# Kernel optimization log

Hardware: AMD Instinct MI355X
Metric: run time of the kernel (lower is better)

## Reference

```python
import jax, jax.numpy as jnp
import numpy as np

E, H, I, T = 8, 1024, 2816, 8192  # experts, hidden, intermediate, total tokens


def setup_inputs() -> dict:
    key = jax.random.key(0)
    k1, k2, k3, k4 = jax.random.split(key, 4)
    x = jax.random.normal(k1, (T, H), dtype=jnp.float32)
    # xavier_normal std = sqrt(2 / (fan_in + fan_out))
    std = (2.0 / (H + I)) ** 0.5
    gate = jax.random.normal(k2, (E, H, I), dtype=jnp.float32) * std
    up = jax.random.normal(k3, (E, H, I), dtype=jnp.float32) * std
    down = jax.random.normal(k4, (E, I, H), dtype=jnp.float32) * std
    # tokens are pre-permuted so each expert's tokens are contiguous; equal split here
    tokens_per_expert = jnp.full((E,), T // E, dtype=jnp.int32)
    return {
        "permuted_local_hidden_states": x,
        "grouped_gate_proj": gate,
        "grouped_up_proj": up,
        "grouped_down_proj": down,
        "tokens_per_expert": tokens_per_expert,
    }


def reference(permuted_local_hidden_states, grouped_gate_proj, grouped_up_proj,
              grouped_down_proj, tokens_per_expert):
    # grouped GEMM: for expert e, rows in its contiguous segment are multiplied by W[e]
    o1 = jax.lax.ragged_dot(permuted_local_hidden_states, grouped_gate_proj,
                            tokens_per_expert)            # [T, I]
    o2 = jax.lax.ragged_dot(permuted_local_hidden_states, grouped_up_proj,
                            tokens_per_expert)            # [T, I]
    inter = jax.nn.silu(o1) * o2                          # SwiGLU  [T, I]
    out = jax.lax.ragged_dot(inter, grouped_down_proj, tokens_per_expert)  # [T, H]
    return out
```

## Files before the change

kernel.cpp:

```cpp
#include <hip/hip_runtime.h>
#include <hip/hip_bf16.h>


#define E_ 8
#define H_ 1024
#define I_ 2816
#define T_ 8192

typedef unsigned short u16;
typedef __attribute__((ext_vector_type(8))) short s16x8;
typedef __attribute__((ext_vector_type(8))) unsigned short u16x8;
typedef __attribute__((ext_vector_type(4))) float f32x4;

__device__ __forceinline__ void async16(const u16* g, u16* l) {
  __builtin_amdgcn_global_load_lds((__attribute__((address_space(1))) void*)g,
                                   (__attribute__((address_space(3))) void*)l, 16, 0, 0);
}

__device__ __forceinline__ u16 f2b(float f) {
  union { __hip_bfloat16 h; u16 u; } c;
  c.h = __float2bfloat16(f);
  return c.u;
}

__global__ __launch_bounds__(256) void convx_k(const float* __restrict__ x,
                                               u16* __restrict__ xb) {
  size_t i = ((size_t)blockIdx.x * 256 + threadIdx.x) * 8;
  float4 v0 = *(const float4*)(x + i);
  float4 v1 = *(const float4*)(x + i + 4);
  u16x8 b;
  b[0] = f2b(v0.x); b[1] = f2b(v0.y); b[2] = f2b(v0.z); b[3] = f2b(v0.w);
  b[4] = f2b(v1.x); b[5] = f2b(v1.y); b[6] = f2b(v1.z); b[7] = f2b(v1.w);
  *(u16x8*)(xb + i) = b;
}

template <int R, int C>
__device__ __forceinline__ void tconv_tile(const float* __restrict__ in,
                                           u16* __restrict__ out,
                                           int bx, int by, int t) {
  __shared__ float tile[64 * 64];
  const int c0 = bx * 64, r0 = by * 64;
  {
    const int rr = t >> 4;
    const int c4 = (t & 15) * 4;
#pragma unroll
    for (int j = 0; j < 4; ++j) {
      const int r = rr + 16 * j;
      float4 v = *(const float4*)(in + (size_t)(r0 + r) * C + c0 + c4);
      tile[r * 64 + ((c4 + 0) ^ r)] = v.x;
      tile[r * 64 + ((c4 + 1) ^ r)] = v.y;
      tile[r * 64 + ((c4 + 2) ^ r)] = v.z;
      tile[r * 64 + ((c4 + 3) ^ r)] = v.w;
    }
  }
  __syncthreads();
  {
    const int c = t >> 2;
    const int rq = (t & 3) * 8;
    u16* o = out + (size_t)(c0 + c) * R + r0;
    u16x8 b;
#pragma unroll
    for (int j = 0; j < 8; ++j) {
      const int r = rq + j;
      b[j] = f2b(tile[r * 64 + (c ^ r)]);
    }
    *(u16x8*)(o + rq) = b;
#pragma unroll
    for (int j = 0; j < 8; ++j) {
      const int r = 32 + rq + j;
      b[j] = f2b(tile[r * 64 + (c ^ r)]);
    }
    *(u16x8*)(o + 32 + rq) = b;
  }
}

__global__ __launch_bounds__(256) void tconvGU_k(const float* __restrict__ G,
                                                 const float* __restrict__ U,
                                                 u16* __restrict__ GT,
                                                 u16* __restrict__ UT) {
  const int z = blockIdx.z;
  const size_t eoff = (size_t)(z >> 1) * (size_t)H_ * I_;
  const float* in = ((z & 1) ? U : G) + eoff;
  u16* out = ((z & 1) ? UT : GT) + eoff;
  tconv_tile<H_, I_>(in, out, blockIdx.x, blockIdx.y, threadIdx.x);
}

__global__ __launch_bounds__(256) void tconvD_k(const float* __restrict__ D,
                                                u16* __restrict__ DT) {
  const size_t eoff = (size_t)blockIdx.z * (size_t)H_ * I_;
  tconv_tile<I_, H_>(D + eoff, DT + eoff, blockIdx.x, blockIdx.y, threadIdx.x);
}

__global__ __launch_bounds__(256, 2) void gemm12_k(
    const u16* __restrict__ X, const u16* __restrict__ GT,
    const u16* __restrict__ UT, const int* __restrict__ tpe,
    u16* __restrict__ inter) {
  __shared__ u16 sA[128 * 32];
  __shared__ u16 sG[64 * 32];
  __shared__ u16 sU[64 * 32];
  const int t = threadIdx.x;
  const int m0 = blockIdx.y * 128;
  const int n0 = blockIdx.x * 64;

  int e = 0, seg_end = T_;
  {
    int s = 0;
    for (int i = 0; i < E_; ++i) {
      int c = tpe[i];
      if (m0 < s + c) { e = i; seg_end = s + c; break; }
      s += c;
    }
  }
  const u16* GTe = GT + (size_t)e * I_ * H_;
  const u16* UTe = UT + (size_t)e * I_ * H_;

  const u16* gA0 = X + (size_t)(m0 + (t >> 2)) * H_ + (t & 3) * 8;
  const u16* gA1 = gA0 + (size_t)64 * H_;
  const u16* gG  = GTe + (size_t)(n0 + (t >> 2)) * H_ + (t & 3) * 8;
  const u16* gU  = UTe + (size_t)(n0 + (t >> 2)) * H_ + (t & 3) * 8;
  u16* lA = sA + t * 8;
  u16* lG = sG + t * 8;
  u16* lU = sU + t * 8;

  const int l = t & 63, w = t >> 6;
  const int wm = (w & 1) * 64, wn = (w >> 1) * 32;
  const u16* fA = sA + (size_t)(wm + (l & 15)) * 32 + (l >> 4) * 8;
  const u16* fG = sG + (size_t)(wn + (l & 15)) * 32 + (l >> 4) * 8;
  const u16* fU = sU + (size_t)(wn + (l & 15)) * 32 + (l >> 4) * 8;

  f32x4 accG[4][2], accU[4][2];
#pragma unroll
  for (int mi = 0; mi < 4; ++mi)
#pragma unroll
    for (int ni = 0; ni < 2; ++ni) {
      accG[mi][ni] = (f32x4){0.f, 0.f, 0.f, 0.f};
      accU[mi][ni] = (f32x4){0.f, 0.f, 0.f, 0.f};
    }

  for (int k0 = 0; k0 < H_; k0 += 32) {
    async16(gA0 + k0, lA);
    async16(gA1 + k0, lA + 2048);
    async16(gG + k0, lG);
    async16(gU + k0, lU);
    __syncthreads();
    s16x8 aF[4], gF[2], uF[2];
#pragma unroll
    for (int mi = 0; mi < 4; ++mi) aF[mi] = *(const s16x8*)(fA + mi * 512);
#pragma unroll
    for (int ni = 0; ni < 2; ++ni) {
      gF[ni] = *(const s16x8*)(fG + ni * 512);
      uF[ni] = *(const s16x8*)(fU + ni * 512);
    }
#pragma unroll
    for (int mi = 0; mi < 4; ++mi)
#pragma unroll
      for (int ni = 0; ni < 2; ++ni) {
        accG[mi][ni] = __builtin_amdgcn_mfma_f32_16x16x32_bf16(aF[mi], gF[ni], accG[mi][ni], 0, 0, 0);
        accU[mi][ni] = __builtin_amdgcn_mfma_f32_16x16x32_bf16(aF[mi], uF[ni], accU[mi][ni], 0, 0, 0);
      }
    __syncthreads();
  }

  const int colb = l & 15, rowb = (l >> 4) * 4;
#pragma unroll
  for (int mi = 0; mi < 4; ++mi)
#pragma unroll
    for (int ni = 0; ni < 2; ++ni) {
      const size_t gcol = (size_t)(n0 + wn + ni * 16 + colb);
#pragma unroll
      for (int r = 0; r < 4; ++r) {
        int grow = m0 + wm + mi * 16 + rowb + r;
        if (grow < seg_end) {
          float o1 = accG[mi][ni][r];
          float o2 = accU[mi][ni][r];
          float sv = o1 / (1.f + __expf(-o1));
          inter[(size_t)grow * I_ + gcol] = f2b(sv * o2);
        }
      }
    }
}

__global__ __launch_bounds__(256, 2) void gemm3_k(
    const u16* __restrict__ A, const u16* __restrict__ DT,
    const int* __restrict__ tpe, float* __restrict__ out) {
  __shared__ u16 sA[128 * 32];
  __shared__ u16 sB[128 * 32];
  const int t = threadIdx.x;
  const int m0 = blockIdx.y * 128;
  const int n0 = blockIdx.x * 128;

  int e = 0, seg_end = T_;
  {
    int s = 0;
    for (int i = 0; i < E_; ++i) {
      int c = tpe[i];
      if (m0 < s + c) { e = i; seg_end = s + c; break; }
      s += c;
    }
  }
  const u16* DTe = DT + (size_t)e * H_ * I_;

  const u16* gA0 = A + (size_t)(m0 + (t >> 2)) * I_ + (t & 3) * 8;
  const u16* gA1 = gA0 + (size_t)64 * I_;
  const u16* gB0 = DTe + (size_t)(n0 + (t >> 2)) * I_ + (t & 3) * 8;
  const u16* gB1 = gB0 + (size_t)64 * I_;
  u16* lA = sA + t * 8;
  u16* lB = sB + t * 8;

  const int l = t & 63, w = t >> 6;
  const int wm = (w & 1) * 64, wn = (w >> 1) * 64;
  const u16* fA = sA + (size_t)(wm + (l & 15)) * 32 + (l >> 4) * 8;
  const u16* fB = sB + (size_t)(wn + (l & 15)) * 32 + (l >> 4) * 8;

  f32x4 acc[4][4];
#pragma unroll
  for (int mi = 0; mi < 4; ++mi)
#pragma unroll
    for (int ni = 0; ni < 4; ++ni) acc[mi][ni] = (f32x4){0.f, 0.f, 0.f, 0.f};

  for (int k0 = 0; k0 < I_; k0 += 32) {
    async16(gA0 + k0, lA);
    async16(gA1 + k0, lA + 2048);
    async16(gB0 + k0, lB);
    async16(gB1 + k0, lB + 2048);
    __syncthreads();
    s16x8 aF[4], bF[4];
#pragma unroll
    for (int mi = 0; mi < 4; ++mi) aF[mi] = *(const s16x8*)(fA + mi * 512);
#pragma unroll
    for (int ni = 0; ni < 4; ++ni) bF[ni] = *(const s16x8*)(fB + ni * 512);
#pragma unroll
    for (int mi = 0; mi < 4; ++mi)
#pragma unroll
      for (int ni = 0; ni < 4; ++ni)
        acc[mi][ni] = __builtin_amdgcn_mfma_f32_16x16x32_bf16(aF[mi], bF[ni], acc[mi][ni], 0, 0, 0);
    __syncthreads();
  }

  const int colb = l & 15, rowb = (l >> 4) * 4;
#pragma unroll
  for (int mi = 0; mi < 4; ++mi)
#pragma unroll
    for (int ni = 0; ni < 4; ++ni) {
      const size_t gcol = (size_t)(n0 + wn + ni * 16 + colb);
#pragma unroll
      for (int r = 0; r < 4; ++r) {
        int grow = m0 + wm + mi * 16 + rowb + r;
        if (grow < seg_end) out[(size_t)grow * H_ + gcol] = acc[mi][ni][r];
      }
    }
}

extern "C" void kernel_launch(void* const* d_in, const int* in_sizes, int n_in,
                              void* d_out, int out_size, void* d_ws, size_t ws_size,
                              hipStream_t stream) {
  const float* X = (const float*)d_in[0];
  const float* G = (const float*)d_in[1];
  const float* U = (const float*)d_in[2];
  const float* D = (const float*)d_in[3];
  const int* tpe = (const int*)d_in[4];
  float* out = (float*)d_out;

  const size_t W = (size_t)E_ * H_ * I_;
  if (ws_size < 3 * W * sizeof(u16)) return;
  u16* r0 = (u16*)d_ws;
  u16* r1 = r0 + W;
  u16* r2 = r1 + W;
  u16* xb = (u16*)d_out;

  convx_k<<<dim3((T_ * H_) / (256 * 8)), 256, 0, stream>>>(X, xb);
  tconvGU_k<<<dim3(I_ / 64, H_ / 64, E_ * 2), 256, 0, stream>>>(G, U, r0, r1);
  gemm12_k<<<dim3(I_ / 64, T_ / 128), 256, 0, stream>>>(xb, r0, r1, tpe, r2);
  tconvD_k<<<dim3(H_ / 64, I_ / 64, E_), 256, 0, stream>>>(D, r0);
  gemm3_k<<<dim3(H_ / 128, T_ / 128), 256, 0, stream>>>(r2, r0, tpe, out);
}
```

Before: 489.5 us.

## Deepen K tiles to 64 with XOR-swizzled LDS and split-K the down GEMM

Both GEMMs now stage 64-wide K tiles in shared memory instead of 32. An XOR swizzle on the column chunk is meant to avoid LDS bank conflicts, and each barrier pair now covers twice the MFMA work. The down-projection GEMM is split into two K halves across blockIdx.z to double the block count (64x8 grid was only 512 blocks). A separate add kernel then sums the partial buffer, which reuses the freed up-proj workspace, into the output. This costs extra fp32 traffic and one more launch.

```diff
diff --git a/kernel.cpp b/kernel.cpp
--- a/kernel.cpp
+++ b/kernel.cpp
@@ -95,9 +95,9 @@
     const u16* __restrict__ X, const u16* __restrict__ GT,
     const u16* __restrict__ UT, const int* __restrict__ tpe,
     u16* __restrict__ inter) {
-  __shared__ u16 sA[128 * 32];
-  __shared__ u16 sG[64 * 32];
-  __shared__ u16 sU[64 * 32];
+  __shared__ u16 sA[128 * 64];
+  __shared__ u16 sG[64 * 64];
+  __shared__ u16 sU[64 * 64];
   const int t = threadIdx.x;
   const int m0 = blockIdx.y * 128;
   const int n0 = blockIdx.x * 64;
@@ -114,19 +114,20 @@
   const u16* GTe = GT + (size_t)e * I_ * H_;
   const u16* UTe = UT + (size_t)e * I_ * H_;
 
-  const u16* gA0 = X + (size_t)(m0 + (t >> 2)) * H_ + (t & 3) * 8;
-  const u16* gA1 = gA0 + (size_t)64 * H_;
-  const u16* gG  = GTe + (size_t)(n0 + (t >> 2)) * H_ + (t & 3) * 8;
-  const u16* gU  = UTe + (size_t)(n0 + (t >> 2)) * H_ + (t & 3) * 8;
+  const int sj = ((t & 7) ^ ((t >> 3) & 7)) * 8;
+  const u16* gA = X + (size_t)(m0 + (t >> 3)) * H_ + sj;
+  const u16* gG = GTe + (size_t)(n0 + (t >> 3)) * H_ + sj;
+  const u16* gU = UTe + (size_t)(n0 + (t >> 3)) * H_ + sj;
   u16* lA = sA + t * 8;
   u16* lG = sG + t * 8;
   u16* lU = sU + t * 8;
 
   const int l = t & 63, w = t >> 6;
   const int wm = (w & 1) * 64, wn = (w >> 1) * 32;
-  const u16* fA = sA + (size_t)(wm + (l & 15)) * 32 + (l >> 4) * 8;
-  const u16* fG = sG + (size_t)(wn + (l & 15)) * 32 + (l >> 4) * 8;
-  const u16* fU = sU + (size_t)(wn + (l & 15)) * 32 + (l >> 4) * 8;
+  const int c0 = (((l >> 4) ^ (l & 7))) * 8;
+  const u16* fA = sA + (size_t)(wm + (l & 15)) * 64;
+  const u16* fG = sG + (size_t)(wn + (l & 15)) * 64;
+  const u16* fU = sU + (size_t)(wn + (l & 15)) * 64;
 
   f32x4 accG[4][2], accU[4][2];
 #pragma unroll
@@ -137,27 +138,35 @@
       accU[mi][ni] = (f32x4){0.f, 0.f, 0.f, 0.f};
     }
 
-  for (int k0 = 0; k0 < H_; k0 += 32) {
-    async16(gA0 + k0, lA);
-    async16(gA1 + k0, lA + 2048);
+  for (int k0 = 0; k0 < H_; k0 += 64) {
+    async16(gA + k0, lA);
+    async16(gA + 32 * H_ + k0, lA + 2048);
+    async16(gA + 64 * H_ + k0, lA + 4096);
+    async16(gA + 96 * H_ + k0, lA + 6144);
     async16(gG + k0, lG);
+    async16(gG + 32 * H_ + k0, lG + 2048);
     async16(gU + k0, lU);
+    async16(gU + 32 * H_ + k0, lU + 2048);
     __syncthreads();
-    s16x8 aF[4], gF[2], uF[2];
-#pragma unroll
-    for (int mi = 0; mi < 4; ++mi) aF[mi] = *(const s16x8*)(fA + mi * 512);
-#pragma unroll
-    for (int ni = 0; ni < 2; ++ni) {
-      gF[ni] = *(const s16x8*)(fG + ni * 512);
-      uF[ni] = *(const s16x8*)(fU + ni * 512);
-    }
-#pragma unroll
-    for (int mi = 0; mi < 4; ++mi)
+#pragma unroll
+    for (int ks = 0; ks < 2; ++ks) {
+      const int co = c0 ^ (ks * 32);
+      s16x8 aF[4], gF[2], uF[2];
+#pragma unroll
+      for (int mi = 0; mi < 4; ++mi) aF[mi] = *(const s16x8*)(fA + mi * 1024 + co);
 #pragma unroll
       for (int ni = 0; ni < 2; ++ni) {
-        accG[mi][ni] = __builtin_amdgcn_mfma_f32_16x16x32_bf16(aF[mi], gF[ni], accG[mi][ni], 0, 0, 0);
-        accU[mi][ni] = __builtin_amdgcn_mfma_f32_16x16x32_bf16(aF[mi], uF[ni], accU[mi][ni], 0, 0, 0);
+        gF[ni] = *(const s16x8*)(fG + ni * 1024 + co);
+        uF[ni] = *(const s16x8*)(fU + ni * 1024 + co);
       }
+#pragma unroll
+      for (int mi = 0; mi < 4; ++mi)
+#pragma unroll
+        for (int ni = 0; ni < 2; ++ni) {
+          accG[mi][ni] = __builtin_amdgcn_mfma_f32_16x16x32_bf16(aF[mi], gF[ni], accG[mi][ni], 0, 0, 0);
+          accU[mi][ni] = __builtin_amdgcn_mfma_f32_16x16x32_bf16(aF[mi], uF[ni], accU[mi][ni], 0, 0, 0);
+        }
+    }
     __syncthreads();
   }
 
@@ -182,12 +191,15 @@
 
 __global__ __launch_bounds__(256, 2) void gemm3_k(
     const u16* __restrict__ A, const u16* __restrict__ DT,
-    const int* __restrict__ tpe, float* __restrict__ out) {
-  __shared__ u16 sA[128 * 32];
-  __shared__ u16 sB[128 * 32];
+    const int* __restrict__ tpe, float* __restrict__ out,
+    float* __restrict__ part) {
+  __shared__ u16 sA[128 * 64];
+  __shared__ u16 sB[128 * 64];
   const int t = threadIdx.x;
   const int m0 = blockIdx.y * 128;
   const int n0 = blockIdx.x * 128;
+  const int ks = blockIdx.z;
+  const int kbase = ks * (I_ / 2);
 
   int e = 0, seg_end = T_;
   {
@@ -200,17 +212,17 @@
   }
   const u16* DTe = DT + (size_t)e * H_ * I_;
 
-  const u16* gA0 = A + (size_t)(m0 + (t >> 2)) * I_ + (t & 3) * 8;
-  const u16* gA1 = gA0 + (size_t)64 * I_;
-  const u16* gB0 = DTe + (size_t)(n0 + (t >> 2)) * I_ + (t & 3) * 8;
-  const u16* gB1 = gB0 + (size_t)64 * I_;
+  const int sj = ((t & 7) ^ ((t >> 3) & 7)) * 8;
+  const u16* gA = A + (size_t)(m0 + (t >> 3)) * I_ + kbase + sj;
+  const u16* gB = DTe + (size_t)(n0 + (t >> 3)) * I_ + kbase + sj;
   u16* lA = sA + t * 8;
   u16* lB = sB + t * 8;
 
   const int l = t & 63, w = t >> 6;
   const int wm = (w & 1) * 64, wn = (w >> 1) * 64;
-  const u16* fA = sA + (size_t)(wm + (l & 15)) * 32 + (l >> 4) * 8;
-  const u16* fB = sB + (size_t)(wn + (l & 15)) * 32 + (l >> 4) * 8;
+  const int c0 = (((l >> 4) ^ (l & 7))) * 8;
+  const u16* fA = sA + (size_t)(wm + (l & 15)) * 64;
+  const u16* fB = sB + (size_t)(wn + (l & 15)) * 64;
 
   f32x4 acc[4][4];
 #pragma unroll
@@ -218,25 +230,34 @@
 #pragma unroll
     for (int ni = 0; ni < 4; ++ni) acc[mi][ni] = (f32x4){0.f, 0.f, 0.f, 0.f};
 
-  for (int k0 = 0; k0 < I_; k0 += 32) {
-    async16(gA0 + k0, lA);
-    async16(gA1 + k0, lA + 2048);
-    async16(gB0 + k0, lB);
-    async16(gB1 + k0, lB + 2048);
+  for (int k0 = 0; k0 < I_ / 2; k0 += 64) {
+    async16(gA + k0, lA);
+    async16(gA + 32 * I_ + k0, lA + 2048);
+    async16(gA + 64 * I_ + k0, lA + 4096);
+    async16(gA + 96 * I_ + k0, lA + 6144);
+    async16(gB + k0, lB);
+    async16(gB + 32 * I_ + k0, lB + 2048);
+    async16(gB + 64 * I_ + k0, lB + 4096);
+    async16(gB + 96 * I_ + k0, lB + 6144);
     __syncthreads();
-    s16x8 aF[4], bF[4];
-#pragma unroll
-    for (int mi = 0; mi < 4; ++mi) aF[mi] = *(const s16x8*)(fA + mi * 512);
-#pragma unroll
-    for (int ni = 0; ni < 4; ++ni) bF[ni] = *(const s16x8*)(fB + ni * 512);
-#pragma unroll
-    for (int mi = 0; mi < 4; ++mi)
-#pragma unroll
-      for (int ni = 0; ni < 4; ++ni)
-        acc[mi][ni] = __builtin_amdgcn_mfma_f32_16x16x32_bf16(aF[mi], bF[ni], acc[mi][ni], 0, 0, 0);
+#pragma unroll
+    for (int kk = 0; kk < 2; ++kk) {
+      const int co = c0 ^ (kk * 32);
+      s16x8 aF[4], bF[4];
+#pragma unroll
+      for (int mi = 0; mi < 4; ++mi) aF[mi] = *(const s16x8*)(fA + mi * 1024 + co);
+#pragma unroll
+      for (int ni = 0; ni < 4; ++ni) bF[ni] = *(const s16x8*)(fB + ni * 1024 + co);
+#pragma unroll
+      for (int mi = 0; mi < 4; ++mi)
+#pragma unroll
+        for (int ni = 0; ni < 4; ++ni)
+          acc[mi][ni] = __builtin_amdgcn_mfma_f32_16x16x32_bf16(aF[mi], bF[ni], acc[mi][ni], 0, 0, 0);
+    }
     __syncthreads();
   }
 
+  float* dst = ks ? part : out;
   const int colb = l & 15, rowb = (l >> 4) * 4;
 #pragma unroll
   for (int mi = 0; mi < 4; ++mi)
@@ -246,9 +267,22 @@
 #pragma unroll
       for (int r = 0; r < 4; ++r) {
         int grow = m0 + wm + mi * 16 + rowb + r;
-        if (grow < seg_end) out[(size_t)grow * H_ + gcol] = acc[mi][ni][r];
+        if (grow < seg_end) dst[(size_t)grow * H_ + gcol] = acc[mi][ni][r];
       }
     }
+}
+
+__global__ __launch_bounds__(256) void add_k(float* __restrict__ out,
+                                             const float* __restrict__ part) {
+  size_t i = ((size_t)blockIdx.x * 256 + threadIdx.x) * 8;
+  float4 a0 = *(float4*)(out + i);
+  float4 a1 = *(float4*)(out + i + 4);
+  float4 b0 = *(const float4*)(part + i);
+  float4 b1 = *(const float4*)(part + i + 4);
+  a0.x += b0.x; a0.y += b0.y; a0.z += b0.z; a0.w += b0.w;
+  a1.x += b1.x; a1.y += b1.y; a1.z += b1.z; a1.w += b1.w;
+  *(float4*)(out + i) = a0;
+  *(float4*)(out + i + 4) = a1;
 }
 
 extern "C" void kernel_launch(void* const* d_in, const int* in_sizes, int n_in,
@@ -267,10 +301,12 @@
   u16* r1 = r0 + W;
   u16* r2 = r1 + W;
   u16* xb = (u16*)d_out;
+  float* part = (float*)r1;
 
   convx_k<<<dim3((T_ * H_) / (256 * 8)), 256, 0, stream>>>(X, xb);
   tconvGU_k<<<dim3(I_ / 64, H_ / 64, E_ * 2), 256, 0, stream>>>(G, U, r0, r1);
   gemm12_k<<<dim3(I_ / 64, T_ / 128), 256, 0, stream>>>(xb, r0, r1, tpe, r2);
   tconvD_k<<<dim3(H_ / 64, I_ / 64, E_), 256, 0, stream>>>(D, r0);
-  gemm3_k<<<dim3(H_ / 128, T_ / 128), 256, 0, stream>>>(r2, r0, tpe, out);
-}
+  gemm3_k<<<dim3(H_ / 128, T_ / 128, 2), 256, 0, stream>>>(r2, r0, tpe, out, part);
+  add_k<<<dim3((T_ * H_) / (256 * 8)), 256, 0, stream>>>(out, part);
+}
```

Measured after the change: 486.6 us. Within noise of the previous version (-0.6%).
